# Kernel optimization log

Hardware: AMD Instinct MI355X
Metric: run time of the kernel (lower is better)

Reference implementation:

```python
import jax, jax.numpy as jnp
import numpy as np

B, N, D = 256, 128, 512
NUM_TYPES, NUM_STATS = 6, 8
W_TYPE, W_STATS, W_CORR = 1.0, 1.0, 0.5
LN_EPS = 1e-5


def setup_inputs() -> dict:
    key = jax.random.key(0)
    ks = jax.random.split(key, 20)
    s = 1.0 / np.sqrt(D)
    inp = {
        "column_embeddings": jax.random.normal(ks[0], (B, N, D), jnp.float32),
        "masked_columns": jax.random.bernoulli(ks[1], 0.15, (B, N)),
        "type_targets": jax.random.randint(ks[2], (N,), 0, NUM_TYPES),
        "column_statistics": jax.random.normal(ks[3], (B, N, NUM_STATS), jnp.float32),
        "column_correlations": jnp.tanh(jax.random.normal(ks[4], (B, N, N), jnp.float32)),
        # type head: Linear(D,D) -> GELU -> LayerNorm -> Linear(D,NUM_TYPES)
        "t_W1": jax.random.normal(ks[5], (D, D), jnp.float32) * s,
        "t_b1": jnp.zeros((D,), jnp.float32),
        "t_g": jnp.ones((D,), jnp.float32),
        "t_beta": jnp.zeros((D,), jnp.float32),
        "t_W2": jax.random.normal(ks[6], (D, NUM_TYPES), jnp.float32) * s,
        "t_b2": jnp.zeros((NUM_TYPES,), jnp.float32),
        # stats head
        "s_W1": jax.random.normal(ks[7], (D, D), jnp.float32) * s,
        "s_b1": jnp.zeros((D,), jnp.float32),
        "s_g": jnp.ones((D,), jnp.float32),
        "s_beta": jnp.zeros((D,), jnp.float32),
        "s_W2": jax.random.normal(ks[8], (D, NUM_STATS), jnp.float32) * s,
        "s_b2": jnp.zeros((NUM_STATS,), jnp.float32),
        # bilinear correlation: x_i^T W x_j + b
        "c_W": jax.random.normal(ks[9], (D, D), jnp.float32) * s,
        "c_b": jnp.zeros((), jnp.float32),
    }
    return inp


def _mlp_head(x, W1, b1, g, beta, W2, b2):
    h = jax.nn.gelu(x @ W1 + b1, approximate=False)
    mu = h.mean(-1, keepdims=True)
    var = ((h - mu) ** 2).mean(-1, keepdims=True)
    h = (h - mu) * jax.lax.rsqrt(var + LN_EPS) * g + beta
    return h @ W2 + b2


def _forward(column_embeddings, masked_columns, type_targets,
             column_statistics, column_correlations,
             t_W1, t_b1, t_g, t_beta, t_W2, t_b2,
             s_W1, s_b1, s_g, s_beta, s_W2, s_b2,
             c_W, c_b):
    e = column_embeddings  # [B,N,D]
    type_logits = _mlp_head(e, t_W1, t_b1, t_g, t_beta, t_W2, t_b2)   # [B,N,T]
    stats_preds = _mlp_head(e, s_W1, s_b1, s_g, s_beta, s_W2, s_b2)   # [B,N,S]

    # batched bilinear correlation: tanh(e_i W e_j + b), diag forced to 1
    u = jnp.einsum('bnd,de->bne', e, c_W)            # [B,N,D]
    corr = jnp.tanh(jnp.einsum('bne,bme->bnm', u, e) + c_b)  # [B,N,N]
    eye = jnp.eye(e.shape[1], dtype=corr.dtype)
    corr = corr * (1.0 - eye) + eye

    m = masked_columns.astype(jnp.float32)           # [B,N]
    n_masked = jnp.maximum(m.sum(), 1.0)

    # type loss: masked-mean cross entropy; targets broadcast over batch
    logp = jax.nn.log_softmax(type_logits, axis=-1)
    tgt = jnp.broadcast_to(type_targets[None, :], m.shape)
    ce = -jnp.take_along_axis(logp, tgt[..., None], axis=-1)[..., 0]  # [B,N]
    type_loss = (ce * m).sum() / n_masked

    # stats loss: masked-mean MSE over [B,N,S]
    se = (stats_preds - column_statistics) ** 2
    stats_loss = (se * m[..., None]).sum() / (n_masked * se.shape[-1])

    # correlation loss: mask_expanded = m_i | m_j
    me = jnp.maximum(m[:, :, None], m[:, None, :])   # [B,N,N]
    n_me = jnp.maximum(me.sum(), 1.0)
    ce2 = (corr - column_correlations) ** 2
    correlation_loss = (ce2 * me).sum() / n_me

    total = W_TYPE * type_loss + W_STATS * stats_loss + W_CORR * correlation_loss
    return total


def reference(column_embeddings, masked_columns, type_targets,
              column_statistics, column_correlations,
              t_W1, t_b1, t_g, t_beta, t_W2, t_b2,
              s_W1, s_b1, s_g, s_beta, s_W2, s_b2,
              c_W, c_b):
    return _forward(column_embeddings, masked_columns, type_targets,
                    column_statistics, column_correlations,
                    t_W1, t_b1, t_g, t_beta, t_W2, t_b2,
                    s_W1, s_b1, s_g, s_beta, s_W2, s_b2,
                    c_W, c_b)
```

## Files before the change

### kernel.cpp

```cpp
#include <hip/hip_runtime.h>
#include <math.h>

#define Bx 256
#define Nx 128
#define Dx 512
#define Mx (Bx * Nx)
#define NTYPES 6
#define NSTATS 8
#define LN_EPS 1e-5f
#define CAP 8192

typedef __attribute__((ext_vector_type(8))) short frag8;
typedef __attribute__((ext_vector_type(4))) float f32x4;

__device__ __forceinline__ unsigned short f2bf(float f) {
    unsigned u = __float_as_uint(f);
    u += 0x7fff + ((u >> 16) & 1);
    return (unsigned short)(u >> 16);
}
__device__ __forceinline__ float bf2f(unsigned short s) {
    return __uint_as_float((unsigned)s << 16);
}

#define ASYNC16(g, l) __builtin_amdgcn_global_load_lds(                      \
    (const __attribute__((address_space(1))) void*)(g),                      \
    (__attribute__((address_space(3))) void*)(l), 16, 0, 0)


#define GSTAGE(b, ph)                                                        \
  {                                                                          \
    ASYNC16(pA0 + (ph) * 32, As + (b) * 4096 + t * 8);                       \
    ASYNC16(pA1 + (ph) * 32, As + (b) * 4096 + 2048 + t * 8);                \
    ASYNC16(pB0 + (ph) * 32, Bs + (b) * 4096 + t * 8);                       \
    ASYNC16(pB1 + (ph) * 32, Bs + (b) * 4096 + 2048 + t * 8);                \
  }

#define GCOMPUTE(pb)                                                         \
  {                                                                          \
    const int lb = (pb) * 4096;                                              \
    frag8 af[4], bfv[4];                                                     \
    _Pragma("unroll") for (int i = 0; i < 4; ++i)                            \
        af[i] = *(const frag8*)&As[lb + (wr + i * 16 + mr) * 32 + co];       \
    _Pragma("unroll") for (int j = 0; j < 4; ++j)                            \
        bfv[j] = *(const frag8*)&Bs[lb + (wcol + j * 16 + mr) * 32 + co];    \
    __builtin_amdgcn_s_setprio(1);                                           \
    _Pragma("unroll") for (int i = 0; i < 4; ++i)                            \
      _Pragma("unroll") for (int j = 0; j < 4; ++j)                          \
        acc[i][j] = __builtin_amdgcn_mfma_f32_16x16x32_bf16(                 \
            af[i], bfv[j], acc[i][j], 0, 0, 0);                              \
    __builtin_amdgcn_s_setprio(0);                                           \
  }

#define GBAR(NIMM)                                                           \
    asm volatile("s_waitcnt vmcnt(" #NIMM ")" ::: "memory");                 \
    __builtin_amdgcn_s_barrier();                                            \
    __builtin_amdgcn_sched_barrier(0);

#define EB_OFF    0ULL
#define U_OFF     33554432ULL
#define HC_OFF    67108864ULL
#define WT_OFF    83886080ULL
#define WTC_OFF   84934656ULL
#define LIST_OFF  85458944ULL
#define CNTS_OFF  85590016ULL
#define PACC_OFF  85591040ULL
#define PCORR_OFF 85593088ULL
#define CNTP_OFF  85594112ULL

__global__ __launch_bounds__(256) void k_prep(
    const float* __restrict__ e, const float* __restrict__ W0,
    const float* __restrict__ W1, const float* __restrict__ W2,
    unsigned short* __restrict__ Eb, unsigned short* __restrict__ Tcmb,
    unsigned short* __restrict__ Tc, const int* __restrict__ m,
    int* __restrict__ list, int* __restrict__ cnts, int* cntp) {
    const int bid = blockIdx.x;
    const int t = threadIdx.x;
    if (bid < 256) {
        const int b = bid;
        const int r = b * Nx + t;
        int v = 0;
        if (t < 128) v = (m[r] != 0) ? 1 : 0;
        const unsigned long long bal = __ballot(v);
        const int wid = t >> 6, lane = t & 63;
        __shared__ int wcnt[2];
        __shared__ int base;
        if (lane == 0 && wid < 2) wcnt[wid] = __popcll(bal);
        __syncthreads();
        const int cnt = wcnt[0] + wcnt[1];
        if (t == 0) {
            base = atomicAdd(cntp, cnt);
            cnts[b] = cnt;
        }
        __syncthreads();
        if (t < 128 && v) {
            const int rank = __popcll(bal & ((1ULL << lane) - 1)) +
                             (wid ? wcnt[0] : 0);
            const int p = base + rank;
            if (p < CAP) list[p] = r;
        }
        return;
    }
    if (bid < 1024) {
        const int lin = (bid - 256) * 256 + t;
        const int mid = lin >> 16;
        const int i4  = (lin & 65535) * 4;
        const int n = i4 >> 9, k = i4 & 511;
        const float* W = (mid == 0) ? W0 : (mid == 1) ? W1 : W2;
        unsigned short* T = (mid == 2) ? Tc : (Tcmb + mid * 262144);
        unsigned short o[4];
#pragma unroll
        for (int j = 0; j < 4; ++j) o[j] = f2bf(W[(k + j) * Dx + n]);
        uint2 u;
        u.x = (unsigned)o[0] | ((unsigned)o[1] << 16);
        u.y = (unsigned)o[2] | ((unsigned)o[3] << 16);
        *(uint2*)(T + i4) = u;
        return;
    }
    const int r = (bid - 1024) * 4 + (t >> 6);
    const int lane = t & 63;
    const float4* src = (const float4*)(e + (size_t)r * Dx);
    const float4 a = src[lane * 2];
    const float4 b = src[lane * 2 + 1];
    unsigned short u[8] = {f2bf(a.x), f2bf(a.y), f2bf(a.z), f2bf(a.w),
                           f2bf(b.x), f2bf(b.y), f2bf(b.z), f2bf(b.w)};
    ((uint4*)(Eb + (size_t)r * Dx))[lane] = *(const uint4*)u;
}

__global__ __launch_bounds__(256) void k_gemms(
    const unsigned short* __restrict__ Eb,
    const unsigned short* __restrict__ Wtc,
    const unsigned short* __restrict__ Wtcmb,
    const float* __restrict__ bias0, const float* __restrict__ bias1,
    unsigned short* __restrict__ U, unsigned short* __restrict__ Hc,
    const int* __restrict__ list, const int* __restrict__ cntp) {
    __shared__ unsigned short As[4 * 4096];
    __shared__ unsigned short Bs[4 * 4096];
    const int bid = blockIdx.x;
    const int t = threadIdx.x;
    const unsigned short* Bbase;
    unsigned short* C;
    int row0, col0, ldc, head, ra0, ra1;
    if (bid < 1024) {
        row0 = ((((bid >> 5) << 3) | (bid & 7))) << 7;
        col0 = ((bid >> 3) & 3) << 7;
        Bbase = Wtc; C = U; ldc = 512; head = 0;
        ra0 = row0 + (t >> 2);
        ra1 = row0 + 64 + (t >> 2);
    } else {
        const int b2 = bid - 1024;
        row0 = (b2 >> 3) << 7;
        const int cnt = min(*cntp, CAP);
        if (row0 >= cnt) return;
        col0 = (b2 & 7) << 7;
        Bbase = Wtcmb; C = Hc; ldc = 1024; head = 1;
        ra0 = list[min(row0 + (t >> 2), cnt - 1)];
        ra1 = list[min(row0 + 64 + (t >> 2), cnt - 1)];
    }
    const int kq = (t & 3) ^ ((t >> 3) & 3);
    const unsigned short* pA0 = Eb + (size_t)ra0 * Dx + kq * 8;
    const unsigned short* pA1 = Eb + (size_t)ra1 * Dx + kq * 8;
    const unsigned short* pB0 = Bbase + (size_t)(col0 + (t >> 2)) * Dx + kq * 8;
    const unsigned short* pB1 = Bbase + (size_t)(col0 + 64 + (t >> 2)) * Dx + kq * 8;

    const int w = t >> 6, l = t & 63;
    const int wr = (w >> 1) * 64, wcol = (w & 1) * 64;
    const int quad = l >> 4, mr = l & 15;
    const int co = (quad ^ ((mr >> 1) & 3)) * 8;

    f32x4 acc[4][4] = {};
    GSTAGE(0, 0); GSTAGE(1, 1); GSTAGE(2, 2);
    for (int p = 0; p < 13; ++p) {
        GBAR(8);
        GSTAGE((p + 3) & 3, p + 3);
        GCOMPUTE(p & 3);
    }
    GBAR(8); GCOMPUTE(1);
    GBAR(4); GCOMPUTE(2);
    GBAR(0); GCOMPUTE(3);

#pragma unroll
    for (int i = 0; i < 4; ++i)
#pragma unroll
        for (int j = 0; j < 4; ++j)
#pragma unroll
            for (int r = 0; r < 4; ++r) {
                const int row = row0 + wr + i * 16 + quad * 4 + r;
                const int col = col0 + wcol + j * 16 + mr;
                float v = acc[i][j][r];
                if (head) {
                    v += (col < 512) ? bias0[col] : bias1[col - 512];
                    v = 0.5f * v * (1.0f + erff(v * 0.70710678118654752f));
                }
                C[(size_t)row * ldc + col] = f2bf(v);
            }
}

__global__ __launch_bounds__(256) void k_tail(
    const unsigned short* __restrict__ U,
    const unsigned short* __restrict__ Eb,
    const float* __restrict__ Ct, const int* __restrict__ m,
    const float* __restrict__ cbp, float* __restrict__ pcorr,
    const unsigned short* __restrict__ Hc,
    const float* __restrict__ tg, const float* __restrict__ tbeta,
    const float* __restrict__ tW2, const float* __restrict__ tb2,
    const float* __restrict__ sg, const float* __restrict__ sbeta,
    const float* __restrict__ sW2, const float* __restrict__ sb2,
    const int* __restrict__ list, const int* __restrict__ cntp,
    const int* __restrict__ tgt, const float* __restrict__ stats,
    float* __restrict__ pacc) {
    __shared__ unsigned short As[4 * 4096];
    __shared__ unsigned short Bs[4 * 4096];
    __shared__ float mloc[128];
    __shared__ float redf[4][2];
    const int t = threadIdx.x;
    const int w = t >> 6, l = t & 63;

    if (blockIdx.x < 256) {
        const int b = blockIdx.x;
        const int wr = (w >> 1) * 64, wcol = (w & 1) * 64;
        const int quad = l >> 4, mr = l & 15;
        const int co = (quad ^ ((mr >> 1) & 3)) * 8;
        if (t < 128) mloc[t] = (m[b * Nx + t] != 0) ? 1.0f : 0.0f;
        asm volatile("s_waitcnt lgkmcnt(0)" ::: "memory");

        const int kq = (t & 3) ^ ((t >> 3) & 3);
        const size_t rb = (size_t)b * Nx;
        const unsigned short* pA0 = U + (rb + (t >> 2)) * Dx + kq * 8;
        const unsigned short* pA1 = U + (rb + 64 + (t >> 2)) * Dx + kq * 8;
        const unsigned short* pB0 = Eb + (rb + (t >> 2)) * Dx + kq * 8;
        const unsigned short* pB1 = Eb + (rb + 64 + (t >> 2)) * Dx + kq * 8;

        f32x4 acc[4][4] = {};
        GSTAGE(0, 0); GSTAGE(1, 1); GSTAGE(2, 2);
        for (int p = 0; p < 13; ++p) {
            GBAR(8);
            GSTAGE((p + 3) & 3, p + 3);
            GCOMPUTE(p & 3);
        }
        GBAR(8); GCOMPUTE(1);
        GBAR(4); GCOMPUTE(2);
        GBAR(0); GCOMPUTE(3);

        const float cb = cbp[0];
        float lsum = 0.0f;
#pragma unroll
        for (int i = 0; i < 4; ++i)
#pragma unroll
            for (int j = 0; j < 4; ++j)
#pragma unroll
                for (int r = 0; r < 4; ++r) {
                    const int row = wr + i * 16 + quad * 4 + r;
                    const int col = wcol + j * 16 + mr;
                    float c = (row == col) ? 1.0f : tanhf(acc[i][j][r] + cb);
                    const float me = fmaxf(mloc[row], mloc[col]);
                    const float d = c - Ct[((size_t)b * Nx + row) * Nx + col];
                    lsum += me * d * d;
                }
#pragma unroll
        for (int off = 32; off > 0; off >>= 1) lsum += __shfl_down(lsum, off);
        if (l == 0) redf[w][0] = lsum;
        __syncthreads();
        if (t == 0) pcorr[b] = redf[0][0] + redf[1][0] + redf[2][0] + redf[3][0];
        return;
    }

    const int blk = blockIdx.x - 256;
    const int cnt = min(*cntp, CAP);
    float ce_acc = 0.0f, sse_acc = 0.0f;
    for (int idx = blk * 4 + w; idx < cnt; idx += 256 * 4) {
        const int r = list[idx];
        const uint4 ut = ((const uint4*)(Hc + (size_t)idx * 1024))[l];
        const uint4 us = ((const uint4*)(Hc + (size_t)idx * 1024 + 512))[l];
        float a[8], b8[8];
        {
            const unsigned uu[4] = {ut.x, ut.y, ut.z, ut.w};
            const unsigned vv[4] = {us.x, us.y, us.z, us.w};
#pragma unroll
            for (int j = 0; j < 4; ++j) {
                a[2 * j]      = bf2f((unsigned short)(uu[j] & 0xffff));
                a[2 * j + 1]  = bf2f((unsigned short)(uu[j] >> 16));
                b8[2 * j]     = bf2f((unsigned short)(vv[j] & 0xffff));
                b8[2 * j + 1] = bf2f((unsigned short)(vv[j] >> 16));
            }
        }
        float st = 0, qt = 0, ss = 0, qs = 0;
#pragma unroll
        for (int j = 0; j < 8; ++j) {
            st += a[j]; qt += a[j] * a[j];
            ss += b8[j]; qs += b8[j] * b8[j];
        }
#pragma unroll
        for (int off = 32; off > 0; off >>= 1) {
            st += __shfl_xor(st, off); qt += __shfl_xor(qt, off);
            ss += __shfl_xor(ss, off); qs += __shfl_xor(qs, off);
        }
        const float mt = st * (1.0f / Dx);
        const float rt = rsqrtf(qt * (1.0f / Dx) - mt * mt + LN_EPS);
        const float ms = ss * (1.0f / Dx);
        const float rs = rsqrtf(qs * (1.0f / Dx) - ms * ms + LN_EPS);

        const int c0 = l * 8;
        float tp[6] = {}, sp[8] = {};
#pragma unroll
        for (int j = 0; j < 8; ++j) {
            const int c = c0 + j;
            const float nt = (a[j] - mt) * rt * tg[c] + tbeta[c];
#pragma unroll
            for (int k = 0; k < 6; ++k) tp[k] += nt * tW2[c * 6 + k];
            const float ns = (b8[j] - ms) * rs * sg[c] + sbeta[c];
#pragma unroll
            for (int k = 0; k < 8; ++k) sp[k] += ns * sW2[c * 8 + k];
        }
#pragma unroll
        for (int k = 0; k < 6; ++k)
#pragma unroll
            for (int off = 32; off > 0; off >>= 1) tp[k] += __shfl_down(tp[k], off);
#pragma unroll
        for (int k = 0; k < 8; ++k)
#pragma unroll
            for (int off = 32; off > 0; off >>= 1) sp[k] += __shfl_down(sp[k], off);

        if (l == 0) {
            float lg[6];
#pragma unroll
            for (int k = 0; k < 6; ++k) lg[k] = tp[k] + tb2[k];
            float mx = lg[0];
#pragma unroll
            for (int k = 1; k < 6; ++k) mx = fmaxf(mx, lg[k]);
            float se = 0.0f;
#pragma unroll
            for (int k = 0; k < 6; ++k) se += expf(lg[k] - mx);
            ce_acc += -(lg[tgt[r & (Nx - 1)]] - mx - logf(se));
            float sse = 0.0f;
#pragma unroll
            for (int k = 0; k < 8; ++k) {
                const float d = sp[k] + sb2[k] - stats[(size_t)r * NSTATS + k];
                sse += d * d;
            }
            sse_acc += sse;
        }
    }
    if (l == 0) { redf[w][0] = ce_acc; redf[w][1] = sse_acc; }
    __syncthreads();
    if (t == 0) {
        pacc[2 * blk]     = redf[0][0] + redf[1][0] + redf[2][0] + redf[3][0];
        pacc[2 * blk + 1] = redf[0][1] + redf[1][1] + redf[2][1] + redf[3][1];
    }
}

__global__ __launch_bounds__(256) void k_final(
    const float* __restrict__ pacc, const float* __restrict__ pcorr,
    const int* __restrict__ cnts, const int* __restrict__ cntp,
    float* __restrict__ out) {
    const int t = threadIdx.x, w = t >> 6, lane = t & 63;
    float ce = pacc[2 * t], sse = pacc[2 * t + 1], co = pcorr[t];
    const int c = cnts[t];
    float me = (float)(Nx * Nx) - (float)((Nx - c) * (Nx - c));
#pragma unroll
    for (int off = 32; off > 0; off >>= 1) {
        ce += __shfl_down(ce, off);
        sse += __shfl_down(sse, off);
        co += __shfl_down(co, off);
        me += __shfl_down(me, off);
    }
    __shared__ float red[4][4];
    if (lane == 0) {
        red[w][0] = ce; red[w][1] = sse; red[w][2] = co; red[w][3] = me;
    }
    __syncthreads();
    if (t == 0) {
        const float CE = red[0][0] + red[1][0] + red[2][0] + red[3][0];
        const float SSE = red[0][1] + red[1][1] + red[2][1] + red[3][1];
        const float CO = red[0][2] + red[1][2] + red[2][2] + red[3][2];
        const float ME = red[0][3] + red[1][3] + red[2][3] + red[3][3];
        const float nm = fmaxf((float)*cntp, 1.0f);
        const float nme = fmaxf(ME, 1.0f);
        out[0] = CE / nm + SSE / (nm * (float)NSTATS) + 0.5f * CO / nme;
    }
}

extern "C" void kernel_launch(void* const* d_in, const int* in_sizes, int n_in,
                              void* d_out, int out_size, void* d_ws, size_t ws_size,
                              hipStream_t stream) {
    const float* e      = (const float*)d_in[0];
    const int*   mcols  = (const int*)d_in[1];
    const int*   ttgt   = (const int*)d_in[2];
    const float* stats  = (const float*)d_in[3];
    const float* corrT  = (const float*)d_in[4];
    const float* tW1    = (const float*)d_in[5];
    const float* tb1    = (const float*)d_in[6];
    const float* tg     = (const float*)d_in[7];
    const float* tbeta  = (const float*)d_in[8];
    const float* tW2    = (const float*)d_in[9];
    const float* tb2    = (const float*)d_in[10];
    const float* sW1    = (const float*)d_in[11];
    const float* sb1    = (const float*)d_in[12];
    const float* sg     = (const float*)d_in[13];
    const float* sbeta  = (const float*)d_in[14];
    const float* sW2    = (const float*)d_in[15];
    const float* sb2    = (const float*)d_in[16];
    const float* cW     = (const float*)d_in[17];
    const float* cb     = (const float*)d_in[18];
    float* out = (float*)d_out;

    char* ws = (char*)d_ws;
    unsigned short* Eb    = (unsigned short*)(ws + EB_OFF);
    unsigned short* U     = (unsigned short*)(ws + U_OFF);
    unsigned short* Hc    = (unsigned short*)(ws + HC_OFF);
    unsigned short* Wtcmb = (unsigned short*)(ws + WT_OFF);
    unsigned short* Wtc   = (unsigned short*)(ws + WTC_OFF);
    int*   list  = (int*)(ws + LIST_OFF);
    int*   cnts  = (int*)(ws + CNTS_OFF);
    float* pacc  = (float*)(ws + PACC_OFF);
    float* pcorr = (float*)(ws + PCORR_OFF);
    int*   cntp  = (int*)(ws + CNTP_OFF);

    hipMemsetAsync(cntp, 0, sizeof(int), stream);
    k_prep<<<9216, 256, 0, stream>>>(e, tW1, sW1, cW, Eb, Wtcmb, Wtc, mcols,
                                     list, cnts, cntp);
    k_gemms<<<1536, 256, 0, stream>>>(Eb, Wtc, Wtcmb, tb1, sb1, U, Hc, list, cntp);
    k_tail<<<512, 256, 0, stream>>>(U, Eb, corrT, mcols, cb, pcorr,
                                    Hc, tg, tbeta, tW2, tb2, sg, sbeta, sW2, sb2,
                                    list, cntp, ttgt, stats, pacc);
    k_final<<<1, 256, 0, stream>>>(pacc, pcorr, cnts, cntp, out);
}
```

Before: 239.9 us.

## Shrink GEMM tiles to single-wave 64x64 blocks and transpose weights via LDS

The bf16 MFMA GEMM kernel goes from 256-thread blocks computing 128x128 tiles with a 4-stage async LDS pipeline to 64-thread single-wave blocks computing 64x64 tiles with double buffering. The grid grows from 1536 to 6144 blocks. Separately, weight transposition in the prep kernel now uses a padded 64x64 shared-memory tile so reads and writes are coalesced, instead of strided 4-element gathers. Smaller tiles raise parallelism and occupancy but halve operand reuse per block and shorten the pipeline, which increases global and LDS traffic per FLOP.

```diff
diff --git a/kernel.cpp b/kernel.cpp
--- a/kernel.cpp
+++ b/kernel.cpp
@@ -26,6 +26,31 @@
     (const __attribute__((address_space(1))) void*)(g),                      \
     (__attribute__((address_space(3))) void*)(l), 16, 0, 0)
 
+#define WSTAGE(buf, k0)                                                      \
+  { _Pragma("unroll") for (int s_ = 0; s_ < 4; ++s_) {                       \
+      ASYNC16(pA[s_] + (k0), As + (buf) * 2048 + s_ * 512 + t * 8);          \
+      ASYNC16(pB[s_] + (k0), Bs + (buf) * 2048 + s_ * 512 + t * 8);          \
+  } }
+
+#define WWAIT(NIMM)                                                          \
+    asm volatile("s_waitcnt vmcnt(" #NIMM ")" ::: "memory");                 \
+    __builtin_amdgcn_sched_barrier(0);
+
+#define WCOMPUTE(pb)                                                         \
+  {                                                                          \
+    const int lb = (pb) * 2048;                                              \
+    frag8 af[4], bfv[4];                                                     \
+    _Pragma("unroll") for (int i = 0; i < 4; ++i)                            \
+        af[i] = *(const frag8*)&As[lb + (i * 16 + mr) * 32 + co];            \
+    _Pragma("unroll") for (int j = 0; j < 4; ++j)                            \
+        bfv[j] = *(const frag8*)&Bs[lb + (j * 16 + mr) * 32 + co];           \
+    __builtin_amdgcn_s_setprio(1);                                           \
+    _Pragma("unroll") for (int i = 0; i < 4; ++i)                            \
+      _Pragma("unroll") for (int j = 0; j < 4; ++j)                          \
+        acc[i][j] = __builtin_amdgcn_mfma_f32_16x16x32_bf16(                 \
+            af[i], bfv[j], acc[i][j], 0, 0, 0);                              \
+    __builtin_amdgcn_s_setprio(0);                                           \
+  }
 
 #define GSTAGE(b, ph)                                                        \
   {                                                                          \
@@ -100,23 +125,30 @@
         }
         return;
     }
-    if (bid < 1024) {
-        const int lin = (bid - 256) * 256 + t;
-        const int mid = lin >> 16;
-        const int i4  = (lin & 65535) * 4;
-        const int n = i4 >> 9, k = i4 & 511;
+    if (bid < 448) {
+        const int lin = bid - 256;
+        const int mid = lin >> 6;
+        const int tl  = lin & 63;
+        const int ti = tl >> 3, tj = tl & 7;
         const float* W = (mid == 0) ? W0 : (mid == 1) ? W1 : W2;
         unsigned short* T = (mid == 2) ? Tc : (Tcmb + mid * 262144);
-        unsigned short o[4];
-#pragma unroll
-        for (int j = 0; j < 4; ++j) o[j] = f2bf(W[(k + j) * Dx + n]);
-        uint2 u;
-        u.x = (unsigned)o[0] | ((unsigned)o[1] << 16);
-        u.y = (unsigned)o[2] | ((unsigned)o[3] << 16);
-        *(uint2*)(T + i4) = u;
+        __shared__ float sh[64][65];
+        const int c = t & 63;
+        const int r4 = t >> 6;
+#pragma unroll
+        for (int rr = 0; rr < 16; ++rr) {
+            const int row = rr * 4 + r4;
+            sh[row][c] = W[(size_t)(ti * 64 + row) * Dx + tj * 64 + c];
+        }
+        __syncthreads();
+#pragma unroll
+        for (int rr = 0; rr < 16; ++rr) {
+            const int col2 = rr * 4 + r4;
+            T[(size_t)(tj * 64 + col2) * Dx + ti * 64 + c] = f2bf(sh[c][col2]);
+        }
         return;
     }
-    const int r = (bid - 1024) * 4 + (t >> 6);
+    const int r = (bid - 448) * 4 + (t >> 6);
     const int lane = t & 63;
     const float4* src = (const float4*)(e + (size_t)r * Dx);
     const float4 a = src[lane * 2];
@@ -126,66 +158,69 @@
     ((uint4*)(Eb + (size_t)r * Dx))[lane] = *(const uint4*)u;
 }
 
-__global__ __launch_bounds__(256) void k_gemms(
+__global__ __launch_bounds__(64) void k_gemms(
     const unsigned short* __restrict__ Eb,
     const unsigned short* __restrict__ Wtc,
     const unsigned short* __restrict__ Wtcmb,
     const float* __restrict__ bias0, const float* __restrict__ bias1,
     unsigned short* __restrict__ U, unsigned short* __restrict__ Hc,
     const int* __restrict__ list, const int* __restrict__ cntp) {
-    __shared__ unsigned short As[4 * 4096];
-    __shared__ unsigned short Bs[4 * 4096];
+    __shared__ unsigned short As[2 * 2048];
+    __shared__ unsigned short Bs[2 * 2048];
     const int bid = blockIdx.x;
     const int t = threadIdx.x;
     const unsigned short* Bbase;
     unsigned short* C;
-    int row0, col0, ldc, head, ra0, ra1;
-    if (bid < 1024) {
-        row0 = ((((bid >> 5) << 3) | (bid & 7))) << 7;
-        col0 = ((bid >> 3) & 3) << 7;
+    int row0, col0, ldc, head;
+    int rowA[4];
+    if (bid < 4096) {
+        row0 = ((((bid >> 6) << 3) | (bid & 7))) << 6;
+        col0 = ((bid >> 3) & 7) << 6;
         Bbase = Wtc; C = U; ldc = 512; head = 0;
-        ra0 = row0 + (t >> 2);
-        ra1 = row0 + 64 + (t >> 2);
+#pragma unroll
+        for (int s = 0; s < 4; ++s) rowA[s] = row0 + s * 16 + (t >> 2);
     } else {
-        const int b2 = bid - 1024;
-        row0 = (b2 >> 3) << 7;
+        const int b2 = bid - 4096;
+        row0 = (b2 >> 4) << 6;
         const int cnt = min(*cntp, CAP);
         if (row0 >= cnt) return;
-        col0 = (b2 & 7) << 7;
+        col0 = (b2 & 15) << 6;
         Bbase = Wtcmb; C = Hc; ldc = 1024; head = 1;
-        ra0 = list[min(row0 + (t >> 2), cnt - 1)];
-        ra1 = list[min(row0 + 64 + (t >> 2), cnt - 1)];
+#pragma unroll
+        for (int s = 0; s < 4; ++s)
+            rowA[s] = list[min(row0 + s * 16 + (t >> 2), cnt - 1)];
     }
     const int kq = (t & 3) ^ ((t >> 3) & 3);
-    const unsigned short* pA0 = Eb + (size_t)ra0 * Dx + kq * 8;
-    const unsigned short* pA1 = Eb + (size_t)ra1 * Dx + kq * 8;
-    const unsigned short* pB0 = Bbase + (size_t)(col0 + (t >> 2)) * Dx + kq * 8;
-    const unsigned short* pB1 = Bbase + (size_t)(col0 + 64 + (t >> 2)) * Dx + kq * 8;
-
-    const int w = t >> 6, l = t & 63;
-    const int wr = (w >> 1) * 64, wcol = (w & 1) * 64;
-    const int quad = l >> 4, mr = l & 15;
+    const unsigned short* pA[4];
+    const unsigned short* pB[4];
+#pragma unroll
+    for (int s = 0; s < 4; ++s) {
+        pA[s] = Eb + (size_t)rowA[s] * Dx + kq * 8;
+        pB[s] = Bbase + (size_t)(col0 + s * 16 + (t >> 2)) * Dx + kq * 8;
+    }
+    const int quad = t >> 4, mr = t & 15;
     const int co = (quad ^ ((mr >> 1) & 3)) * 8;
 
     f32x4 acc[4][4] = {};
-    GSTAGE(0, 0); GSTAGE(1, 1); GSTAGE(2, 2);
-    for (int p = 0; p < 13; ++p) {
-        GBAR(8);
-        GSTAGE((p + 3) & 3, p + 3);
-        GCOMPUTE(p & 3);
-    }
-    GBAR(8); GCOMPUTE(1);
-    GBAR(4); GCOMPUTE(2);
-    GBAR(0); GCOMPUTE(3);
-
+    WSTAGE(0, 0);
+#pragma unroll
+    for (int k = 0; k < 16; ++k) {
+        if (k < 15) {
+            WSTAGE((k + 1) & 1, (k + 1) * 32);
+            WWAIT(8);
+        } else {
+            WWAIT(0);
+        }
+        WCOMPUTE(k & 1);
+    }
 #pragma unroll
     for (int i = 0; i < 4; ++i)
 #pragma unroll
         for (int j = 0; j < 4; ++j)
 #pragma unroll
             for (int r = 0; r < 4; ++r) {
-                const int row = row0 + wr + i * 16 + quad * 4 + r;
-                const int col = col0 + wcol + j * 16 + mr;
+                const int row = row0 + i * 16 + quad * 4 + r;
+                const int col = col0 + j * 16 + mr;
                 float v = acc[i][j][r];
                 if (head) {
                     v += (col < 512) ? bias0[col] : bias1[col - 512];
@@ -416,9 +451,9 @@
     int*   cntp  = (int*)(ws + CNTP_OFF);
 
     hipMemsetAsync(cntp, 0, sizeof(int), stream);
-    k_prep<<<9216, 256, 0, stream>>>(e, tW1, sW1, cW, Eb, Wtcmb, Wtc, mcols,
+    k_prep<<<8640, 256, 0, stream>>>(e, tW1, sW1, cW, Eb, Wtcmb, Wtc, mcols,
                                      list, cnts, cntp);
-    k_gemms<<<1536, 256, 0, stream>>>(Eb, Wtc, Wtcmb, tb1, sb1, U, Hc, list, cntp);
+    k_gemms<<<6144, 64, 0, stream>>>(Eb, Wtc, Wtcmb, tb1, sb1, U, Hc, list, cntp);
     k_tail<<<512, 256, 0, stream>>>(U, Eb, corrT, mcols, cb, pcorr,
                                     Hc, tg, tbeta, tW2, tb2, sg, sbeta, sW2, sb2,
                                     list, cntp, ttgt, stats, pacc);
```

Result: no change. 244.1 us (+1.7%).
